# Performance work log

Hardware: AMD Instinct MI355X
Metric: run time of the kernel (lower is better)

The kernel has to match this reference:

```python
import jax, jax.numpy as jnp
import numpy as np

L = 96
K = 3  # conv kernel size

def setup_inputs() -> dict:
    key = jax.random.key(0)
    ks = jax.random.split(key, 6)
    linear_x = jax.random.randint(ks[0], (4 * L**3,), 0, 2, dtype=jnp.int32)
    tetraeder_2 = jax.random.normal(ks[1], (2, 2), dtype=jnp.float32)
    w1 = jax.random.normal(ks[2], (K, K, K, 12, 16), dtype=jnp.float32) * 0.05
    b1 = jnp.zeros((16,), dtype=jnp.float32)
    w2 = jax.random.normal(ks[3], (K, K, K, 16, 32), dtype=jnp.float32) * 0.05
    b2 = jnp.zeros((32,), dtype=jnp.float32)
    wd = jax.random.normal(ks[4], (32, 1), dtype=jnp.float32) * 0.1
    return {"linear_x": linear_x, "tetraeder_2": tetraeder_2,
            "w1": w1, "b1": b1, "w2": w2, "b2": b2, "wd": wd}

def _bonds(linear_x, tetraeder_2):
    # x: (L,L,L,4) spin config; v: (L,L,L,4,d) per-site vectors via gather
    x = linear_x.reshape(L, L, L, 4)
    v = tetraeder_2[x]
    v0, v1, v2, v3 = v[..., 0, :], v[..., 1, :], v[..., 2, :], v[..., 3, :]
    # roll(v, 1, ax)[a] == v[(a-1) % L] -> periodic neighbor cells cell_1/2/3
    r1 = jnp.roll(v1, 1, axis=0)
    r2 = jnp.roll(v2, 1, axis=1)
    r3 = jnp.roll(v3, 1, axis=2)
    dot = lambda a, b: jnp.einsum('...d,...d->...', a, b)
    # 12 bonds in the exact order of on_unit_cell
    bonds = [dot(v0, v1), dot(v0, v2), dot(v0, v3),
             dot(v0, r1), dot(v0, r2), dot(v0, r3),
             dot(v1, v2), dot(v2, v3), dot(v3, v1),
             dot(r1, r2), dot(r2, r3), dot(r3, r1)]
    return jnp.stack(bonds, axis=-1)  # (L,L,L,12)

def _conv_block(y, w, b):
    pad = [(0, 0)] + [((K - 1) // 2, K // 2)] * 3 + [(0, 0)]
    y = jnp.pad(y, pad, mode='wrap')
    y = jax.lax.conv_general_dilated(
        y, w, window_strides=(1, 1, 1), padding='VALID',
        dimension_numbers=('NDHWC', 'DHWIO', 'NDHWC'))
    return jax.nn.elu(y + b)

def reference(linear_x, tetraeder_2, w1, b1, w2, b2, wd):
    y = _bonds(linear_x, tetraeder_2)[jnp.newaxis, ...]  # (1,L,L,L,12)
    y = _conv_block(y, w1, b1)
    y = _conv_block(y, w2, b2)
    y = jnp.mean(y, axis=(1, 2, 3)).ravel()  # (32,)
    return (y @ wd).ravel()[0]
```

## Files before the change

### kernel.cpp

```cpp
#include <hip/hip_runtime.h>
#include <hip/hip_bf16.h>
#include <cmath>

#define L 96
#define L3 (L*L*L)
#define NCONV 3456

#define BSTRIDE 456

typedef __attribute__((ext_vector_type(8))) short short8;
typedef __attribute__((ext_vector_type(4))) float floatx4;

__device__ __forceinline__ float eluf(float x) {
    float e = __expf(x) - 1.0f;
    return x > 0.0f ? x : e;
}

__device__ __forceinline__ unsigned short f2bf(float f) {
    __hip_bfloat16 h = __float2bfloat16(f);
    return *reinterpret_cast<unsigned short*>(&h);
}

__device__ __forceinline__ int wrapc(int x) {
    if (x < 0) x += L;
    if (x >= L) x -= L;
    return x;
}

__global__ __launch_bounds__(256) void wconv_kernel(
    const float* __restrict__ w1, const float* __restrict__ w2,
    unsigned short* __restrict__ Bm1, unsigned short* __restrict__ Bm2)
{
    int idx = blockIdx.x * 256 + threadIdx.x;
    if (idx < 16*448) {
        int o = idx / 448, k = idx % 448;
        int tau = k >> 4, i = k & 15;
        float v = (tau < 27 && i < 12) ? w1[tau*192 + i*16 + o] : 0.0f;
        Bm1[o*448 + k] = f2bf(v);
    }
    int j = idx - 16*448;
    if (j >= 0 && j < 32*448) {
        int o = j / 448, k = j % 448;
        int tau = k >> 4;
        int i = k & 15;
        float v = (tau < 27) ? w2[tau*512 + i*32 + o] : 0.0f;
        Bm2[o*448 + k] = f2bf(v);
    }
}

__global__ __launch_bounds__(256) void bonds_kernel(
    const int* __restrict__ lx, const float* __restrict__ tet,
    unsigned short* __restrict__ bnd)
{
    int idx = blockIdx.x * 256 + threadIdx.x;
    int w = idx % L;
    int t = idx / L;
    int h = t % L;
    int d = t / L;

    float t00 = tet[0], t01 = tet[1], t10 = tet[2], t11 = tet[3];
    float d00 = t00*t00 + t01*t01;
    float d01 = t00*t10 + t01*t11;
    float d11 = t10*t10 + t11*t11;

    const int4 sv = *reinterpret_cast<const int4*>(lx + 4*idx);
    int s0 = sv.x, s1 = sv.y, s2 = sv.z, s3 = sv.w;
    int dm = (d == 0) ? L-1 : d-1;
    int hm = (h == 0) ? L-1 : h-1;
    int wm = (w == 0) ? L-1 : w-1;
    int r1 = lx[4*((dm*L + h)*L + w) + 1];
    int r2 = lx[4*((d*L + hm)*L + w) + 2];
    int r3 = lx[4*((d*L + h)*L + wm) + 3];

    auto dot = [&](int a, int b) -> float {
        return (a == b) ? (a ? d11 : d00) : d01;
    };

    union { unsigned short s[16]; int4 q[2]; } u;
    u.s[0]  = f2bf(dot(s0, s1));
    u.s[1]  = f2bf(dot(s0, s2));
    u.s[2]  = f2bf(dot(s0, s3));
    u.s[3]  = f2bf(dot(s0, r1));
    u.s[4]  = f2bf(dot(s0, r2));
    u.s[5]  = f2bf(dot(s0, r3));
    u.s[6]  = f2bf(dot(s1, s2));
    u.s[7]  = f2bf(dot(s2, s3));
    u.s[8]  = f2bf(dot(s3, s1));
    u.s[9]  = f2bf(dot(r1, r2));
    u.s[10] = f2bf(dot(r2, r3));
    u.s[11] = f2bf(dot(r3, r1));
    u.s[12] = 0; u.s[13] = 0; u.s[14] = 0; u.s[15] = 0;

    int4* dst = reinterpret_cast<int4*>(bnd + (size_t)idx*16);
    dst[0] = u.q[0];
    dst[1] = u.q[1];
}

__device__ __forceinline__ void stage_tile(
    const unsigned short* __restrict__ x, unsigned short* __restrict__ tile,
    int W0, int H0, int D0, int tid)
{
    #pragma unroll
    for (int i = 0; i < 6; ++i) {
        int t = tid + i*256;
        if (i < 5 || t < 1296) {
            int row = t / 36, off = t - row*36;
            int dd = row / 6, hh = row - dd*6;
            int gd = wrapc(D0 + dd - 1);
            int gh = wrapc(H0 + hh - 1);
            int vox = off >> 1, half = off & 1;
            int gw = wrapc(W0 + vox - 1);
            size_t gi = ((size_t)((gd*L + gh)*L + gw))*16 + half*8;
            __builtin_amdgcn_global_load_lds(
                (const __attribute__((address_space(1))) unsigned int*)(x + gi),
                (__attribute__((address_space(3))) unsigned int*)(tile + t*8),
                16, 0, 0);
        }
    }
}

__global__ __launch_bounds__(256, 4) void conv1_kernel(
    const unsigned short* __restrict__ x, const unsigned short* __restrict__ Bm,
    const float* __restrict__ bias, unsigned short* __restrict__ y)
{
    __shared__ unsigned short tile[6*6*18*16];
    __shared__ unsigned short Bls[16*BSTRIDE];
    int tid = threadIdx.x;
    int W0 = blockIdx.x * 16, H0 = blockIdx.y * 4, D0 = blockIdx.z * 4;

    stage_tile(x, tile, W0, H0, D0, tid);
    #pragma unroll
    for (int i = 0; i < 4; ++i) {
        int t = tid + i*256;
        if (i < 3 || t < 896) {
            int row = t / 56, col = t - row*56;
            *reinterpret_cast<int4*>(&Bls[row*BSTRIDE + col*8]) =
                *reinterpret_cast<const int4*>(&Bm[row*448 + col*8]);
        }
    }
    __syncthreads();

    int lane = tid & 63, wave = tid >> 6;
    int laneV = lane & 15, g = lane >> 4;

    floatx4 acc[4];
    #pragma unroll
    for (int m = 0; m < 4; ++m) acc[m] = (floatx4)(0.0f);

    int moff[4];
    #pragma unroll
    for (int m = 0; m < 4; ++m) {
        int mt = wave*4 + m;
        moff[m] = (((mt >> 2)*6 + (mt & 3))*18)*16;
    }

    auto aoff_of = [&](int kt) {
        int tau = 2*kt + (g >> 1);
        if (tau > 26) tau = 26;
        int kd = tau / 9;
        int r  = tau - kd*9;
        int kh = r / 3;
        int kw = r - kh*3;
        return ((kd*6 + kh)*18 + kw + laneV)*16 + (g & 1)*8;
    };

    short8 aC[4], aN[4], bC, bN;
    {
        int a0 = aoff_of(0);
        bC = *reinterpret_cast<const short8*>(&Bls[laneV*BSTRIDE + g*8]);
        #pragma unroll
        for (int m = 0; m < 4; ++m)
            aC[m] = *reinterpret_cast<const short8*>(&tile[moff[m] + a0]);
    }

    #pragma unroll
    for (int kt = 0; kt < 14; ++kt) {
        if (kt < 13) {
            int an = aoff_of(kt+1);
            bN = *reinterpret_cast<const short8*>(&Bls[laneV*BSTRIDE + (kt+1)*32 + g*8]);
            #pragma unroll
            for (int m = 0; m < 4; ++m)
                aN[m] = *reinterpret_cast<const short8*>(&tile[moff[m] + an]);
        }
        #pragma unroll
        for (int m = 0; m < 4; ++m)
            acc[m] = __builtin_amdgcn_mfma_f32_16x16x32_bf16(aC[m], bC, acc[m], 0, 0, 0);
        if (kt < 13) {
            #pragma unroll
            for (int m = 0; m < 4; ++m) aC[m] = aN[m];
            bC = bN;
        }
    }

    float bch = bias[laneV];
    #pragma unroll
    for (int m = 0; m < 4; ++m) {
        int mt = wave*4 + m;
        int d = D0 + (mt >> 2), h = H0 + (mt & 3);
        int wb = W0 + g*4;
        size_t base = ((size_t)((d*L + h)*L + wb))*16 + laneV;
        #pragma unroll
        for (int reg = 0; reg < 4; ++reg) {
            y[base + (size_t)reg*16] = f2bf(eluf(acc[m][reg] + bch));
        }
    }
}

__global__ __launch_bounds__(256, 4) void conv2_kernel(
    const unsigned short* __restrict__ x, const unsigned short* __restrict__ Bm,
    const float* __restrict__ bias, const float* __restrict__ wd,
    float* __restrict__ partials)
{
    __shared__ unsigned short tile[6*6*18*16];
    __shared__ unsigned short Bls[32*BSTRIDE];
    __shared__ float red[4];
    int tid = threadIdx.x;
    int W0 = blockIdx.x * 16, H0 = blockIdx.y * 4, D0 = blockIdx.z * 4;

    stage_tile(x, tile, W0, H0, D0, tid);
    #pragma unroll
    for (int i = 0; i < 7; ++i) {
        int t = tid + i*256;
        int row = t / 56, col = t - row*56;
        *reinterpret_cast<int4*>(&Bls[row*BSTRIDE + col*8]) =
            *reinterpret_cast<const int4*>(&Bm[row*448 + col*8]);
    }
    __syncthreads();

    int lane = tid & 63, wave = tid >> 6;
    int laneV = lane & 15, g = lane >> 4;

    floatx4 acc[4][2];
    #pragma unroll
    for (int m = 0; m < 4; ++m) {
        acc[m][0] = (floatx4)(0.0f);
        acc[m][1] = (floatx4)(0.0f);
    }

    int moff[4];
    #pragma unroll
    for (int m = 0; m < 4; ++m) {
        int mt = wave*4 + m;
        moff[m] = (((mt >> 2)*6 + (mt & 3))*18)*16;
    }

    auto aoff_of = [&](int kt) {
        int tau = 2*kt + (g >> 1);
        if (tau > 26) tau = 26;
        int kd = tau / 9;
        int r  = tau - kd*9;
        int kh = r / 3;
        int kw = r - kh*3;
        return ((kd*6 + kh)*18 + kw + laneV)*16 + (g & 1)*8;
    };

    short8 aC[4], aN[4], bC0, bC1, bN0, bN1;
    {
        int a0 = aoff_of(0);
        bC0 = *reinterpret_cast<const short8*>(&Bls[laneV*BSTRIDE + g*8]);
        bC1 = *reinterpret_cast<const short8*>(&Bls[(16 + laneV)*BSTRIDE + g*8]);
        #pragma unroll
        for (int m = 0; m < 4; ++m)
            aC[m] = *reinterpret_cast<const short8*>(&tile[moff[m] + a0]);
    }

    #pragma unroll
    for (int kt = 0; kt < 14; ++kt) {
        if (kt < 13) {
            int an = aoff_of(kt+1);
            bN0 = *reinterpret_cast<const short8*>(&Bls[laneV*BSTRIDE + (kt+1)*32 + g*8]);
            bN1 = *reinterpret_cast<const short8*>(&Bls[(16 + laneV)*BSTRIDE + (kt+1)*32 + g*8]);
            #pragma unroll
            for (int m = 0; m < 4; ++m)
                aN[m] = *reinterpret_cast<const short8*>(&tile[moff[m] + an]);
        }
        #pragma unroll
        for (int m = 0; m < 4; ++m) {
            acc[m][0] = __builtin_amdgcn_mfma_f32_16x16x32_bf16(aC[m], bC0, acc[m][0], 0, 0, 0);
            acc[m][1] = __builtin_amdgcn_mfma_f32_16x16x32_bf16(aC[m], bC1, acc[m][1], 0, 0, 0);
        }
        if (kt < 13) {
            #pragma unroll
            for (int m = 0; m < 4; ++m) aC[m] = aN[m];
            bC0 = bN0; bC1 = bN1;
        }
    }

    float b2a = bias[laneV], b2b = bias[16 + laneV];
    float wda = wd[laneV],  wdb = wd[16 + laneV];
    float s = 0.0f;
    #pragma unroll
    for (int m = 0; m < 4; ++m) {
        #pragma unroll
        for (int reg = 0; reg < 4; ++reg) {
            s += eluf(acc[m][0][reg] + b2a) * wda;
            s += eluf(acc[m][1][reg] + b2b) * wdb;
        }
    }

    #pragma unroll
    for (int off = 32; off; off >>= 1) s += __shfl_down(s, off);
    if (lane == 0) red[wave] = s;
    __syncthreads();
    if (tid == 0) {
        int bid = (blockIdx.z * gridDim.y + blockIdx.y) * gridDim.x + blockIdx.x;
        partials[bid] = red[0] + red[1] + red[2] + red[3];
    }
}

__global__ __launch_bounds__(256) void final_kernel(
    const float* __restrict__ partials, float* __restrict__ out)
{
    float s = 0.0f;
    for (int i = threadIdx.x; i < NCONV; i += 256) s += partials[i];
    #pragma unroll
    for (int off = 32; off; off >>= 1) s += __shfl_down(s, off);
    __shared__ float red[4];
    int lane = threadIdx.x & 63;
    int wv   = threadIdx.x >> 6;
    if (lane == 0) red[wv] = s;
    __syncthreads();
    if (threadIdx.x == 0)
        out[0] = (red[0] + red[1] + red[2] + red[3]) * (1.0f / (float)L3);
}

extern "C" void kernel_launch(void* const* d_in, const int* in_sizes, int n_in,
                              void* d_out, int out_size, void* d_ws, size_t ws_size,
                              hipStream_t stream) {
    const int*   lx  = (const int*)  d_in[0];
    const float* tet = (const float*)d_in[1];
    const float* w1  = (const float*)d_in[2];
    const float* b1  = (const float*)d_in[3];
    const float* w2  = (const float*)d_in[4];
    const float* b2  = (const float*)d_in[5];
    const float* wd  = (const float*)d_in[6];
    float* out = (float*)d_out;

    char* ws = (char*)d_ws;
    const size_t ARR_BYTES = (size_t)L3 * 16 * 2;
    unsigned short* bnd  = (unsigned short*)ws;
    unsigned short* y1   = (unsigned short*)(ws + ARR_BYTES);
    unsigned short* Bm1  = (unsigned short*)(ws + 2*ARR_BYTES);
    unsigned short* Bm2  = (unsigned short*)(ws + 2*ARR_BYTES + 16*448*2);
    float* partials      = (float*)         (ws + 2*ARR_BYTES + 48*448*2);

    wconv_kernel<<<84, 256, 0, stream>>>(w1, w2, Bm1, Bm2);
    bonds_kernel<<<L3/256, 256, 0, stream>>>(lx, tet, bnd);
    conv1_kernel<<<dim3(6,24,24), 256, 0, stream>>>(bnd, Bm1, b1, y1);
    conv2_kernel<<<dim3(6,24,24), 256, 0, stream>>>(y1, Bm2, b2, wd, partials);
    final_kernel<<<1, 256, 0, stream>>>(partials, out);
}
```

Before: 161.0 us.

## Loop each conv block over four depth tiles with double-buffered LDS staging

Both conv kernels now walk four consecutive depth tiles per block instead of one. The grid shrinks by four along z and the partials count drops to match. While the MFMA loop computes the current tile, the async global-to-LDS load of the next tile is issued into a second LDS buffer. The weight matrix is staged once per block. The aim is to hide the tile-load latency behind compute and amortize weight staging, at the cost of doubled tile LDS, launch bounds lowered to 2 blocks, and fewer blocks to spread across CUs.

```diff
diff --git a/kernel.cpp b/kernel.cpp
--- a/kernel.cpp
+++ b/kernel.cpp
@@ -4,7 +4,8 @@
 
 #define L 96
 #define L3 (L*L*L)
-#define NCONV 3456
+#define TT 4
+#define NPART 864
 
 #define BSTRIDE 456
 
@@ -97,7 +98,7 @@
 }
 
 __device__ __forceinline__ void stage_tile(
-    const unsigned short* __restrict__ x, unsigned short* __restrict__ tile,
+    const unsigned short* __restrict__ x, unsigned short* __restrict__ tbuf,
     int W0, int H0, int D0, int tid)
 {
     #pragma unroll
@@ -113,22 +114,22 @@
             size_t gi = ((size_t)((gd*L + gh)*L + gw))*16 + half*8;
             __builtin_amdgcn_global_load_lds(
                 (const __attribute__((address_space(1))) unsigned int*)(x + gi),
-                (__attribute__((address_space(3))) unsigned int*)(tile + t*8),
+                (__attribute__((address_space(3))) unsigned int*)(tbuf + t*8),
                 16, 0, 0);
         }
     }
 }
 
-__global__ __launch_bounds__(256, 4) void conv1_kernel(
+__global__ __launch_bounds__(256, 2) void conv1_kernel(
     const unsigned short* __restrict__ x, const unsigned short* __restrict__ Bm,
     const float* __restrict__ bias, unsigned short* __restrict__ y)
 {
-    __shared__ unsigned short tile[6*6*18*16];
+    __shared__ unsigned short tile[2][6*6*18*16];
     __shared__ unsigned short Bls[16*BSTRIDE];
     int tid = threadIdx.x;
-    int W0 = blockIdx.x * 16, H0 = blockIdx.y * 4, D0 = blockIdx.z * 4;
-
-    stage_tile(x, tile, W0, H0, D0, tid);
+    int W0 = blockIdx.x * 16, H0 = blockIdx.y * 4;
+    int Dbase = blockIdx.z * (4*TT);
+
     #pragma unroll
     for (int i = 0; i < 4; ++i) {
         int t = tid + i*256;
@@ -138,14 +139,10 @@
                 *reinterpret_cast<const int4*>(&Bm[row*448 + col*8]);
         }
     }
-    __syncthreads();
+    stage_tile(x, tile[0], W0, H0, Dbase, tid);
 
     int lane = tid & 63, wave = tid >> 6;
     int laneV = lane & 15, g = lane >> 4;
-
-    floatx4 acc[4];
-    #pragma unroll
-    for (int m = 0; m < 4; ++m) acc[m] = (floatx4)(0.0f);
 
     int moff[4];
     #pragma unroll
@@ -153,7 +150,6 @@
         int mt = wave*4 + m;
         moff[m] = (((mt >> 2)*6 + (mt & 3))*18)*16;
     }
-
     auto aoff_of = [&](int kt) {
         int tau = 2*kt + (g >> 1);
         if (tau > 26) tau = 26;
@@ -163,61 +159,72 @@
         int kw = r - kh*3;
         return ((kd*6 + kh)*18 + kw + laneV)*16 + (g & 1)*8;
     };
-
-    short8 aC[4], aN[4], bC, bN;
-    {
-        int a0 = aoff_of(0);
-        bC = *reinterpret_cast<const short8*>(&Bls[laneV*BSTRIDE + g*8]);
-        #pragma unroll
-        for (int m = 0; m < 4; ++m)
-            aC[m] = *reinterpret_cast<const short8*>(&tile[moff[m] + a0]);
-    }
-
-    #pragma unroll
-    for (int kt = 0; kt < 14; ++kt) {
-        if (kt < 13) {
-            int an = aoff_of(kt+1);
-            bN = *reinterpret_cast<const short8*>(&Bls[laneV*BSTRIDE + (kt+1)*32 + g*8]);
+    float bch = bias[laneV];
+
+    for (int t = 0; t < TT; ++t) {
+        __syncthreads();
+        if (t + 1 < TT)
+            stage_tile(x, tile[(t+1)&1], W0, H0, Dbase + (t+1)*4, tid);
+
+        const unsigned short* tb = tile[t&1];
+        floatx4 acc[4];
+        #pragma unroll
+        for (int m = 0; m < 4; ++m) acc[m] = (floatx4)(0.0f);
+
+        short8 aC[4], aN[4], bC, bN;
+        {
+            int a0 = aoff_of(0);
+            bC = *reinterpret_cast<const short8*>(&Bls[laneV*BSTRIDE + g*8]);
             #pragma unroll
             for (int m = 0; m < 4; ++m)
-                aN[m] = *reinterpret_cast<const short8*>(&tile[moff[m] + an]);
-        }
-        #pragma unroll
-        for (int m = 0; m < 4; ++m)
-            acc[m] = __builtin_amdgcn_mfma_f32_16x16x32_bf16(aC[m], bC, acc[m], 0, 0, 0);
-        if (kt < 13) {
-            #pragma unroll
-            for (int m = 0; m < 4; ++m) aC[m] = aN[m];
-            bC = bN;
-        }
-    }
-
-    float bch = bias[laneV];
-    #pragma unroll
-    for (int m = 0; m < 4; ++m) {
-        int mt = wave*4 + m;
-        int d = D0 + (mt >> 2), h = H0 + (mt & 3);
-        int wb = W0 + g*4;
-        size_t base = ((size_t)((d*L + h)*L + wb))*16 + laneV;
-        #pragma unroll
-        for (int reg = 0; reg < 4; ++reg) {
-            y[base + (size_t)reg*16] = f2bf(eluf(acc[m][reg] + bch));
-        }
-    }
-}
-
-__global__ __launch_bounds__(256, 4) void conv2_kernel(
+                aC[m] = *reinterpret_cast<const short8*>(&tb[moff[m] + a0]);
+        }
+        #pragma unroll
+        for (int kt = 0; kt < 14; ++kt) {
+            if (kt < 13) {
+                int an = aoff_of(kt+1);
+                bN = *reinterpret_cast<const short8*>(&Bls[laneV*BSTRIDE + (kt+1)*32 + g*8]);
+                #pragma unroll
+                for (int m = 0; m < 4; ++m)
+                    aN[m] = *reinterpret_cast<const short8*>(&tb[moff[m] + an]);
+            }
+            #pragma unroll
+            for (int m = 0; m < 4; ++m)
+                acc[m] = __builtin_amdgcn_mfma_f32_16x16x32_bf16(aC[m], bC, acc[m], 0, 0, 0);
+            if (kt < 13) {
+                #pragma unroll
+                for (int m = 0; m < 4; ++m) aC[m] = aN[m];
+                bC = bN;
+            }
+        }
+
+        int D0 = Dbase + t*4;
+        #pragma unroll
+        for (int m = 0; m < 4; ++m) {
+            int mt = wave*4 + m;
+            int d = D0 + (mt >> 2), h = H0 + (mt & 3);
+            int wb = W0 + g*4;
+            size_t base = ((size_t)((d*L + h)*L + wb))*16 + laneV;
+            #pragma unroll
+            for (int reg = 0; reg < 4; ++reg) {
+                y[base + (size_t)reg*16] = f2bf(eluf(acc[m][reg] + bch));
+            }
+        }
+    }
+}
+
+__global__ __launch_bounds__(256, 2) void conv2_kernel(
     const unsigned short* __restrict__ x, const unsigned short* __restrict__ Bm,
     const float* __restrict__ bias, const float* __restrict__ wd,
     float* __restrict__ partials)
 {
-    __shared__ unsigned short tile[6*6*18*16];
+    __shared__ unsigned short tile[2][6*6*18*16];
     __shared__ unsigned short Bls[32*BSTRIDE];
     __shared__ float red[4];
     int tid = threadIdx.x;
-    int W0 = blockIdx.x * 16, H0 = blockIdx.y * 4, D0 = blockIdx.z * 4;
-
-    stage_tile(x, tile, W0, H0, D0, tid);
+    int W0 = blockIdx.x * 16, H0 = blockIdx.y * 4;
+    int Dbase = blockIdx.z * (4*TT);
+
     #pragma unroll
     for (int i = 0; i < 7; ++i) {
         int t = tid + i*256;
@@ -225,17 +232,10 @@
         *reinterpret_cast<int4*>(&Bls[row*BSTRIDE + col*8]) =
             *reinterpret_cast<const int4*>(&Bm[row*448 + col*8]);
     }
-    __syncthreads();
+    stage_tile(x, tile[0], W0, H0, Dbase, tid);
 
     int lane = tid & 63, wave = tid >> 6;
     int laneV = lane & 15, g = lane >> 4;
-
-    floatx4 acc[4][2];
-    #pragma unroll
-    for (int m = 0; m < 4; ++m) {
-        acc[m][0] = (floatx4)(0.0f);
-        acc[m][1] = (floatx4)(0.0f);
-    }
 
     int moff[4];
     #pragma unroll
@@ -243,7 +243,6 @@
         int mt = wave*4 + m;
         moff[m] = (((mt >> 2)*6 + (mt & 3))*18)*16;
     }
-
     auto aoff_of = [&](int kt) {
         int tau = 2*kt + (g >> 1);
         if (tau > 26) tau = 26;
@@ -253,48 +252,61 @@
         int kw = r - kh*3;
         return ((kd*6 + kh)*18 + kw + laneV)*16 + (g & 1)*8;
     };
-
-    short8 aC[4], aN[4], bC0, bC1, bN0, bN1;
-    {
-        int a0 = aoff_of(0);
-        bC0 = *reinterpret_cast<const short8*>(&Bls[laneV*BSTRIDE + g*8]);
-        bC1 = *reinterpret_cast<const short8*>(&Bls[(16 + laneV)*BSTRIDE + g*8]);
-        #pragma unroll
-        for (int m = 0; m < 4; ++m)
-            aC[m] = *reinterpret_cast<const short8*>(&tile[moff[m] + a0]);
-    }
-
-    #pragma unroll
-    for (int kt = 0; kt < 14; ++kt) {
-        if (kt < 13) {
-            int an = aoff_of(kt+1);
-            bN0 = *reinterpret_cast<const short8*>(&Bls[laneV*BSTRIDE + (kt+1)*32 + g*8]);
-            bN1 = *reinterpret_cast<const short8*>(&Bls[(16 + laneV)*BSTRIDE + (kt+1)*32 + g*8]);
-            #pragma unroll
-            for (int m = 0; m < 4; ++m)
-                aN[m] = *reinterpret_cast<const short8*>(&tile[moff[m] + an]);
-        }
-        #pragma unroll
-        for (int m = 0; m < 4; ++m) {
-            acc[m][0] = __builtin_amdgcn_mfma_f32_16x16x32_bf16(aC[m], bC0, acc[m][0], 0, 0, 0);
-            acc[m][1] = __builtin_amdgcn_mfma_f32_16x16x32_bf16(aC[m], bC1, acc[m][1], 0, 0, 0);
-        }
-        if (kt < 13) {
-            #pragma unroll
-            for (int m = 0; m < 4; ++m) aC[m] = aN[m];
-            bC0 = bN0; bC1 = bN1;
-        }
-    }
-
     float b2a = bias[laneV], b2b = bias[16 + laneV];
     float wda = wd[laneV],  wdb = wd[16 + laneV];
+
     float s = 0.0f;
-    #pragma unroll
-    for (int m = 0; m < 4; ++m) {
-        #pragma unroll
-        for (int reg = 0; reg < 4; ++reg) {
-            s += eluf(acc[m][0][reg] + b2a) * wda;
-            s += eluf(acc[m][1][reg] + b2b) * wdb;
+    for (int t = 0; t < TT; ++t) {
+        __syncthreads();
+        if (t + 1 < TT)
+            stage_tile(x, tile[(t+1)&1], W0, H0, Dbase + (t+1)*4, tid);
+
+        const unsigned short* tb = tile[t&1];
+        floatx4 acc[4][2];
+        #pragma unroll
+        for (int m = 0; m < 4; ++m) {
+            acc[m][0] = (floatx4)(0.0f);
+            acc[m][1] = (floatx4)(0.0f);
+        }
+
+        short8 aC[4], aN[4], bC0, bC1, bN0, bN1;
+        {
+            int a0 = aoff_of(0);
+            bC0 = *reinterpret_cast<const short8*>(&Bls[laneV*BSTRIDE + g*8]);
+            bC1 = *reinterpret_cast<const short8*>(&Bls[(16 + laneV)*BSTRIDE + g*8]);
+            #pragma unroll
+            for (int m = 0; m < 4; ++m)
+                aC[m] = *reinterpret_cast<const short8*>(&tb[moff[m] + a0]);
+        }
+        #pragma unroll
+        for (int kt = 0; kt < 14; ++kt) {
+            if (kt < 13) {
+                int an = aoff_of(kt+1);
+                bN0 = *reinterpret_cast<const short8*>(&Bls[laneV*BSTRIDE + (kt+1)*32 + g*8]);
+                bN1 = *reinterpret_cast<const short8*>(&Bls[(16 + laneV)*BSTRIDE + (kt+1)*32 + g*8]);
+                #pragma unroll
+                for (int m = 0; m < 4; ++m)
+                    aN[m] = *reinterpret_cast<const short8*>(&tb[moff[m] + an]);
+            }
+            #pragma unroll
+            for (int m = 0; m < 4; ++m) {
+                acc[m][0] = __builtin_amdgcn_mfma_f32_16x16x32_bf16(aC[m], bC0, acc[m][0], 0, 0, 0);
+                acc[m][1] = __builtin_amdgcn_mfma_f32_16x16x32_bf16(aC[m], bC1, acc[m][1], 0, 0, 0);
+            }
+            if (kt < 13) {
+                #pragma unroll
+                for (int m = 0; m < 4; ++m) aC[m] = aN[m];
+                bC0 = bN0; bC1 = bN1;
+            }
+        }
+
+        #pragma unroll
+        for (int m = 0; m < 4; ++m) {
+            #pragma unroll
+            for (int reg = 0; reg < 4; ++reg) {
+                s += eluf(acc[m][0][reg] + b2a) * wda;
+                s += eluf(acc[m][1][reg] + b2b) * wdb;
+            }
         }
     }
 
@@ -312,7 +324,7 @@
     const float* __restrict__ partials, float* __restrict__ out)
 {
     float s = 0.0f;
-    for (int i = threadIdx.x; i < NCONV; i += 256) s += partials[i];
+    for (int i = threadIdx.x; i < NPART; i += 256) s += partials[i];
     #pragma unroll
     for (int off = 32; off; off >>= 1) s += __shfl_down(s, off);
     __shared__ float red[4];
@@ -346,7 +358,7 @@
 
     wconv_kernel<<<84, 256, 0, stream>>>(w1, w2, Bm1, Bm2);
     bonds_kernel<<<L3/256, 256, 0, stream>>>(lx, tet, bnd);
-    conv1_kernel<<<dim3(6,24,24), 256, 0, stream>>>(bnd, Bm1, b1, y1);
-    conv2_kernel<<<dim3(6,24,24), 256, 0, stream>>>(y1, Bm2, b2, wd, partials);
+    conv1_kernel<<<dim3(6,24,6), 256, 0, stream>>>(bnd, Bm1, b1, y1);
+    conv2_kernel<<<dim3(6,24,6), 256, 0, stream>>>(y1, Bm2, b2, wd, partials);
     final_kernel<<<1, 256, 0, stream>>>(partials, out);
 }
```

Result: slower. 167.8 us (+4.2%).

## Fuse bond computation into conv1 tile staging, drop bonds kernel

Applied to the files above, without the earlier changes.

Removes the separate bonds kernel and its 28 MB bf16 intermediate array. Conv1 now computes the 12 bond features for its haloed tile straight from the spin integers and writes them into LDS. This saves a kernel launch plus a global write and read of the bond tensor. In exchange, halo voxels (6x6x18 per 4x4x16 output tile) are recomputed and each reads four spin ints, including three neighbour loads, with synchronous loads instead of async global-to-LDS copies.

```diff
diff --git a/kernel.cpp b/kernel.cpp
--- a/kernel.cpp
+++ b/kernel.cpp
@@ -46,54 +46,6 @@
         float v = (tau < 27) ? w2[tau*512 + i*32 + o] : 0.0f;
         Bm2[o*448 + k] = f2bf(v);
     }
-}
-
-__global__ __launch_bounds__(256) void bonds_kernel(
-    const int* __restrict__ lx, const float* __restrict__ tet,
-    unsigned short* __restrict__ bnd)
-{
-    int idx = blockIdx.x * 256 + threadIdx.x;
-    int w = idx % L;
-    int t = idx / L;
-    int h = t % L;
-    int d = t / L;
-
-    float t00 = tet[0], t01 = tet[1], t10 = tet[2], t11 = tet[3];
-    float d00 = t00*t00 + t01*t01;
-    float d01 = t00*t10 + t01*t11;
-    float d11 = t10*t10 + t11*t11;
-
-    const int4 sv = *reinterpret_cast<const int4*>(lx + 4*idx);
-    int s0 = sv.x, s1 = sv.y, s2 = sv.z, s3 = sv.w;
-    int dm = (d == 0) ? L-1 : d-1;
-    int hm = (h == 0) ? L-1 : h-1;
-    int wm = (w == 0) ? L-1 : w-1;
-    int r1 = lx[4*((dm*L + h)*L + w) + 1];
-    int r2 = lx[4*((d*L + hm)*L + w) + 2];
-    int r3 = lx[4*((d*L + h)*L + wm) + 3];
-
-    auto dot = [&](int a, int b) -> float {
-        return (a == b) ? (a ? d11 : d00) : d01;
-    };
-
-    union { unsigned short s[16]; int4 q[2]; } u;
-    u.s[0]  = f2bf(dot(s0, s1));
-    u.s[1]  = f2bf(dot(s0, s2));
-    u.s[2]  = f2bf(dot(s0, s3));
-    u.s[3]  = f2bf(dot(s0, r1));
-    u.s[4]  = f2bf(dot(s0, r2));
-    u.s[5]  = f2bf(dot(s0, r3));
-    u.s[6]  = f2bf(dot(s1, s2));
-    u.s[7]  = f2bf(dot(s2, s3));
-    u.s[8]  = f2bf(dot(s3, s1));
-    u.s[9]  = f2bf(dot(r1, r2));
-    u.s[10] = f2bf(dot(r2, r3));
-    u.s[11] = f2bf(dot(r3, r1));
-    u.s[12] = 0; u.s[13] = 0; u.s[14] = 0; u.s[15] = 0;
-
-    int4* dst = reinterpret_cast<int4*>(bnd + (size_t)idx*16);
-    dst[0] = u.q[0];
-    dst[1] = u.q[1];
 }
 
 __device__ __forceinline__ void stage_tile(
@@ -120,15 +72,15 @@
 }
 
 __global__ __launch_bounds__(256, 4) void conv1_kernel(
-    const unsigned short* __restrict__ x, const unsigned short* __restrict__ Bm,
-    const float* __restrict__ bias, unsigned short* __restrict__ y)
+    const int* __restrict__ lx, const float* __restrict__ tet,
+    const unsigned short* __restrict__ Bm, const float* __restrict__ bias,
+    unsigned short* __restrict__ y)
 {
     __shared__ unsigned short tile[6*6*18*16];
     __shared__ unsigned short Bls[16*BSTRIDE];
     int tid = threadIdx.x;
     int W0 = blockIdx.x * 16, H0 = blockIdx.y * 4, D0 = blockIdx.z * 4;
 
-    stage_tile(x, tile, W0, H0, D0, tid);
     #pragma unroll
     for (int i = 0; i < 4; ++i) {
         int t = tid + i*256;
@@ -136,6 +88,55 @@
             int row = t / 56, col = t - row*56;
             *reinterpret_cast<int4*>(&Bls[row*BSTRIDE + col*8]) =
                 *reinterpret_cast<const int4*>(&Bm[row*448 + col*8]);
+        }
+    }
+
+    float t00 = tet[0], t01 = tet[1], t10 = tet[2], t11 = tet[3];
+    float d00 = t00*t00 + t01*t01;
+    float d01 = t00*t10 + t01*t11;
+    float d11 = t10*t10 + t11*t11;
+
+    #pragma unroll
+    for (int r = 0; r < 3; ++r) {
+        int v = tid + r*256;
+        if (r < 2 || v < 648) {
+            int row = v / 18, vox = v - row*18;
+            int dd = row / 6, hh = row - dd*6;
+            int gd = wrapc(D0 + dd - 1);
+            int gh = wrapc(H0 + hh - 1);
+            int gw = wrapc(W0 + vox - 1);
+            int idx = (gd*L + gh)*L + gw;
+            const int4 sv = *reinterpret_cast<const int4*>(lx + 4*idx);
+            int s0 = sv.x, s1 = sv.y, s2 = sv.z, s3 = sv.w;
+            int dm = wrapc(gd - 1);
+            int hm = wrapc(gh - 1);
+            int wm = wrapc(gw - 1);
+            int r1 = lx[4*((dm*L + gh)*L + gw) + 1];
+            int r2 = lx[4*((gd*L + hm)*L + gw) + 2];
+            int r3 = lx[4*((gd*L + gh)*L + wm) + 3];
+
+            auto dot = [&](int a, int b) -> float {
+                return (a == b) ? (a ? d11 : d00) : d01;
+            };
+
+            union { unsigned short s[16]; int4 q[2]; } u;
+            u.s[0]  = f2bf(dot(s0, s1));
+            u.s[1]  = f2bf(dot(s0, s2));
+            u.s[2]  = f2bf(dot(s0, s3));
+            u.s[3]  = f2bf(dot(s0, r1));
+            u.s[4]  = f2bf(dot(s0, r2));
+            u.s[5]  = f2bf(dot(s0, r3));
+            u.s[6]  = f2bf(dot(s1, s2));
+            u.s[7]  = f2bf(dot(s2, s3));
+            u.s[8]  = f2bf(dot(s3, s1));
+            u.s[9]  = f2bf(dot(r1, r2));
+            u.s[10] = f2bf(dot(r2, r3));
+            u.s[11] = f2bf(dot(r3, r1));
+            u.s[12] = 0; u.s[13] = 0; u.s[14] = 0; u.s[15] = 0;
+
+            int4* dst = reinterpret_cast<int4*>(&tile[row*288 + vox*16]);
+            dst[0] = u.q[0];
+            dst[1] = u.q[1];
         }
     }
     __syncthreads();
@@ -338,15 +339,13 @@
 
     char* ws = (char*)d_ws;
     const size_t ARR_BYTES = (size_t)L3 * 16 * 2;
-    unsigned short* bnd  = (unsigned short*)ws;
-    unsigned short* y1   = (unsigned short*)(ws + ARR_BYTES);
-    unsigned short* Bm1  = (unsigned short*)(ws + 2*ARR_BYTES);
-    unsigned short* Bm2  = (unsigned short*)(ws + 2*ARR_BYTES + 16*448*2);
-    float* partials      = (float*)         (ws + 2*ARR_BYTES + 48*448*2);
+    unsigned short* y1   = (unsigned short*)ws;
+    unsigned short* Bm1  = (unsigned short*)(ws + ARR_BYTES);
+    unsigned short* Bm2  = (unsigned short*)(ws + ARR_BYTES + 16*448*2);
+    float* partials      = (float*)         (ws + ARR_BYTES + 48*448*2);
 
     wconv_kernel<<<84, 256, 0, stream>>>(w1, w2, Bm1, Bm2);
-    bonds_kernel<<<L3/256, 256, 0, stream>>>(lx, tet, bnd);
-    conv1_kernel<<<dim3(6,24,24), 256, 0, stream>>>(bnd, Bm1, b1, y1);
+    conv1_kernel<<<dim3(6,24,24), 256, 0, stream>>>(lx, tet, Bm1, b1, y1);
     conv2_kernel<<<dim3(6,24,24), 256, 0, stream>>>(y1, Bm2, b2, wd, partials);
     final_kernel<<<1, 256, 0, stream>>>(partials, out);
 }
```

Result: slower. 179.5 us (+11.5%).
